# Kernel tuning notes

Measured on AMD Instinct MI355X. Metric: run time of the kernel, lower is better.

The kernel has to match this reference:

```python
import jax, jax.numpy as jnp
import numpy as np

DT = 0.1  # Euler timestep (init kwarg)

def setup_inputs() -> dict:
    key = jax.random.key(0)
    ks = jax.random.split(key, 6)
    B, L, S, U, H = 1024, 512, 64, 32, 512
    return {
        "initial_state": jax.random.normal(ks[0], (B, S), dtype=jnp.float32),
        "control_inputs": jax.random.normal(ks[1], (B, L, U), dtype=jnp.float32),
        "W1": jax.random.normal(ks[2], (S + U, H), dtype=jnp.float32) * (1.0 / np.sqrt(S + U)),
        "b1": jnp.zeros((H,), dtype=jnp.float32),
        "W2": jax.random.normal(ks[3], (H, S), dtype=jnp.float32) * (1.0 / np.sqrt(H)),
        "b2": jnp.zeros((S,), dtype=jnp.float32),
    }

def reference(initial_state, control_inputs, W1, b1, W2, b2):
    # Euler integration: state_{t+1} = state_t + dt * f(state_t, u_t)
    # f is a 2-layer tanh MLP on the concatenated [state, control].
    def step(state, u):
        z = jnp.concatenate([state, u], axis=-1)        # (B, S+U)
        diff = jnp.tanh(z @ W1 + b1) @ W2 + b2          # (B, S)
        new_state = state + diff * DT
        return new_state, new_state

    u_seq = jnp.swapaxes(control_inputs, 0, 1)          # (L, B, U)
    _, states = jax.lax.scan(step, initial_state, u_seq)  # (L, B, S)
    return jnp.swapaxes(states, 0, 1)                   # (B, L, S)
```

## Files before the change

### kernel.cpp

```cpp
#include <hip/hip_runtime.h>
#include <hip/hip_fp16.h>


typedef _Float16 f16;
typedef __attribute__((ext_vector_type(2))) _Float16 f16x2;
typedef __attribute__((ext_vector_type(8))) _Float16 f16x8;
typedef __attribute__((ext_vector_type(2))) float f32x2;
typedef __attribute__((ext_vector_type(4))) float f32x4;

#define MFMA16(a, b, c) __builtin_amdgcn_mfma_f32_16x16x32_f16((a), (b), (c), 0, 0, 0)

__device__ __forceinline__ f16x2 pkrtz(float a, float b) {
    return __builtin_bit_cast(f16x2, __builtin_amdgcn_cvt_pkrtz(a, b));
}

__device__ __forceinline__ float tanh_fast(float x) {
    float t = __builtin_amdgcn_exp2f(x * 2.885390081777927f);
    float r = __builtin_amdgcn_rcpf(t + 1.0f);
    return __builtin_fmaf(-2.0f, r, 1.0f);
}

__global__ __launch_bounds__(512, 1)
void euler_kernel(const float* __restrict__ init,
                  const float* __restrict__ uin,
                  const float* __restrict__ W1,
                  const float* __restrict__ b1,
                  const float* __restrict__ W2,
                  const float* __restrict__ b2,
                  float* __restrict__ out) {
    const int L = 512, S = 64, U = 32, H = 512;
    const int tid  = threadIdx.x;
    const int lane = tid & 63;
    const int w    = tid >> 6;
    const int g    = lane >> 4;
    const int r16  = lane & 15;
    const int b0   = blockIdx.x * 16;

    __shared__ f16   zbuf[256 * 8];
    __shared__ float pbuf[8 * 1024];

    f16x8 W1F[4][4];
    f16x8 W1Fu[2][4];
    #pragma unroll
    for (int kk = 0; kk < 6; ++kk)
      #pragma unroll
      for (int nf = 0; nf < 4; ++nf) {
          const int hcol = w * 64 + 32 * (nf >> 1) + 8 * (r16 >> 2) + 4 * (nf & 1) + (r16 & 3);
          #pragma unroll
          for (int j = 0; j < 8; ++j) {
              int k  = kk * 32 + g * 8 + j;
              int kr = (k < 128) ? (k & 63) : (64 + (k & 31));
              f16 v  = (f16)W1[kr * H + hcol];
              if (kk < 4) W1F[kk][nf][j] = v; else W1Fu[kk - 4][nf][j] = v;
          }
      }
    f32x4 b1v[4];
    #pragma unroll
    for (int nf = 0; nf < 4; ++nf)
        b1v[nf] = *(const f32x4*)&b1[w * 64 + 32 * (nf >> 1) + 4 * (nf & 1) + 8 * g];

    f16x8 W2F[2][4];
    #pragma unroll
    for (int a = 0; a < 2; ++a)
      #pragma unroll
      for (int ns = 0; ns < 4; ++ns)
        #pragma unroll
        for (int j = 0; j < 8; ++j) {
            int k = w * 64 + a * 32 + g * 8 + j;
            W2F[a][ns][j] = (f16)W2[k * S + ns * 16 + r16];
        }

    const int l5 = lane >> 5, r = lane & 31;
    const int sP = (w >> 1) * 16 + (r >> 1);
    const int bP = ((w & 1) * 2 + l5) * 4 + 2 * (r & 1);
    const float b2v = b2[sP];
    const int zci = ((sP >> 5) * 64 + ((sP >> 3) & 3) * 16 + bP) * 8 + (sP & 7);

    f32x2 stateF;
    stateF[0] = init[(size_t)(b0 + bP) * S + sP];
    stateF[1] = init[(size_t)(b0 + bP + 1) * S + sP];
    {
        f16x2 sh = pkrtz(stateF[0], stateF[1]);
        f16x2 sl = pkrtz(stateF[0] - (float)sh[0], stateF[1] - (float)sh[1]);
        zbuf[zci]            = sh[0];
        zbuf[zci + 8]        = sh[1];
        zbuf[zci + 1024]     = sl[0];
        zbuf[zci + 1024 + 8] = sl[1];
    }

    const float* uptr = uin + (size_t)(b0 + r16) * L * U + g * 8;
    f32x4 ua0 = *(const f32x4*)uptr;
    f32x4 ua1 = *(const f32x4*)(uptr + 4);
    f32x4 uacc[4];
    #pragma unroll
    for (int nf = 0; nf < 4; ++nf) uacc[nf] = b1v[nf];
    {
        f16x2 a01 = pkrtz(ua0[0], ua0[1]), a23 = pkrtz(ua0[2], ua0[3]);
        f16x2 c01 = pkrtz(ua1[0], ua1[1]), c23 = pkrtz(ua1[2], ua1[3]);
        f16x2 la  = pkrtz(ua0[0] - (float)a01[0], ua0[1] - (float)a01[1]);
        f16x2 lb  = pkrtz(ua0[2] - (float)a23[0], ua0[3] - (float)a23[1]);
        f16x2 lc  = pkrtz(ua1[0] - (float)c01[0], ua1[1] - (float)c01[1]);
        f16x2 ld  = pkrtz(ua1[2] - (float)c23[0], ua1[3] - (float)c23[1]);
        f16x8 uh, ul;
        uh[0]=a01[0]; uh[1]=a01[1]; uh[2]=a23[0]; uh[3]=a23[1];
        uh[4]=c01[0]; uh[5]=c01[1]; uh[6]=c23[0]; uh[7]=c23[1];
        ul[0]=la[0];  ul[1]=la[1];  ul[2]=lb[0];  ul[3]=lb[1];
        ul[4]=lc[0];  ul[5]=lc[1];  ul[6]=ld[0];  ul[7]=ld[1];
        #pragma unroll
        for (int nf = 0; nf < 4; ++nf) uacc[nf] = MFMA16(W1Fu[0][nf], uh, uacc[nf]);
        #pragma unroll
        for (int nf = 0; nf < 4; ++nf) uacc[nf] = MFMA16(W1Fu[1][nf], ul, uacc[nf]);
    }
    ua0 = *(const f32x4*)(uptr + U);
    ua1 = *(const f32x4*)(uptr + U + 4);
    __syncthreads();

    #pragma unroll 1
    for (int t = 0; t < L; ++t) {
        f16x8 zf[4];
        #pragma unroll
        for (int kk = 0; kk < 4; ++kk)
            zf[kk] = *(const f16x8*)&zbuf[(kk * 64 + lane) * 8];
        #pragma unroll
        for (int kk = 0; kk < 4; ++kk)
          #pragma unroll
          for (int nf = 0; nf < 4; ++nf)
            uacc[nf] = MFMA16(W1F[kk][nf], zf[kk], uacc[nf]);
        f16x8 hb[2];
        #pragma unroll
        for (int a = 0; a < 2; ++a)
          #pragma unroll
          for (int j8 = 0; j8 < 8; ++j8) {
              int nf = a * 2 + (j8 >> 2), jj = j8 & 3;
              hb[a][j8] = (f16)tanh_fast(uacc[nf][jj]);
          }
        f32x4 acc2[4];
        #pragma unroll
        for (int ns = 0; ns < 4; ++ns) acc2[ns] = (f32x4){0.f, 0.f, 0.f, 0.f};
        #pragma unroll
        for (int a = 0; a < 2; ++a)
          #pragma unroll
          for (int ns = 0; ns < 4; ++ns)
            acc2[ns] = MFMA16(hb[a], W2F[a][ns], acc2[ns]);
        #pragma unroll
        for (int ns = 0; ns < 4; ++ns)
            *(f32x4*)&pbuf[(w * 256 + ns * 64 + lane) * 4] = acc2[ns];

        #pragma unroll
        for (int nf = 0; nf < 4; ++nf) uacc[nf] = b1v[nf];
        {
            f16x2 a01 = pkrtz(ua0[0], ua0[1]), a23 = pkrtz(ua0[2], ua0[3]);
            f16x2 c01 = pkrtz(ua1[0], ua1[1]), c23 = pkrtz(ua1[2], ua1[3]);
            f16x2 la  = pkrtz(ua0[0] - (float)a01[0], ua0[1] - (float)a01[1]);
            f16x2 lb  = pkrtz(ua0[2] - (float)a23[0], ua0[3] - (float)a23[1]);
            f16x2 lc  = pkrtz(ua1[0] - (float)c01[0], ua1[1] - (float)c01[1]);
            f16x2 ld  = pkrtz(ua1[2] - (float)c23[0], ua1[3] - (float)c23[1]);
            f16x8 uh, ul;
            uh[0]=a01[0]; uh[1]=a01[1]; uh[2]=a23[0]; uh[3]=a23[1];
            uh[4]=c01[0]; uh[5]=c01[1]; uh[6]=c23[0]; uh[7]=c23[1];
            ul[0]=la[0];  ul[1]=la[1];  ul[2]=lb[0];  ul[3]=lb[1];
            ul[4]=lc[0];  ul[5]=lc[1];  ul[6]=ld[0];  ul[7]=ld[1];
            #pragma unroll
            for (int nf = 0; nf < 4; ++nf) uacc[nf] = MFMA16(W1Fu[0][nf], uh, uacc[nf]);
            #pragma unroll
            for (int nf = 0; nf < 4; ++nf) uacc[nf] = MFMA16(W1Fu[1][nf], ul, uacc[nf]);
        }
        {
            int tp = (t + 2 < L) ? (t + 2) : (L - 1);
            ua0 = *(const f32x4*)(uptr + (size_t)tp * U);
            ua1 = *(const f32x4*)(uptr + (size_t)tp * U + 4);
        }
        __syncthreads();

        f32x2 p[8];
        #pragma unroll
        for (int ww = 0; ww < 8; ++ww)
            p[ww] = *(const f32x2*)&pbuf[ww * 1024 + w * 128 + lane * 2];

        f32x2 s01 = (f32x2){0.f, 0.f}, s23 = s01, s45 = s01, s67 = s01;
        #pragma unroll
        for (int j = 0; j < 2; ++j) {
            s01[j] = p[0][j] + p[1][j];
            s23[j] = p[2][j] + p[3][j];
            s45[j] = p[4][j] + p[5][j];
            s67[j] = p[6][j] + p[7][j];
        }
        float d0 = ((s01[0] + s23[0]) + (s45[0] + s67[0])) + b2v;
        float d1 = ((s01[1] + s23[1]) + (s45[1] + s67[1])) + b2v;
        float sn0 = __builtin_fmaf(0.1f, d0, stateF[0]);
        float sn1 = __builtin_fmaf(0.1f, d1, stateF[1]);
        stateF[0] = sn0; stateF[1] = sn1;
        f16x2 sh = pkrtz(sn0, sn1);
        f16x2 sl = pkrtz(sn0 - (float)sh[0], sn1 - (float)sh[1]);
        zbuf[zci]            = sh[0];
        zbuf[zci + 8]        = sh[1];
        zbuf[zci + 1024]     = sl[0];
        zbuf[zci + 1024 + 8] = sl[1];
        out[((size_t)(b0 + bP) * L + t) * S + sP]     = sn0;
        out[((size_t)(b0 + bP + 1) * L + t) * S + sP] = sn1;
        __syncthreads();
    }
}

extern "C" void kernel_launch(void* const* d_in, const int* in_sizes, int n_in,
                              void* d_out, int out_size, void* d_ws, size_t ws_size,
                              hipStream_t stream) {
    const float* init = (const float*)d_in[0];
    const float* uin  = (const float*)d_in[1];
    const float* W1   = (const float*)d_in[2];
    const float* b1   = (const float*)d_in[3];
    const float* W2   = (const float*)d_in[4];
    const float* b2   = (const float*)d_in[5];
    euler_kernel<<<dim3(64), dim3(512), 0, stream>>>(init, uin, W1, b1, W2, b2,
                                                     (float*)d_out);
}
```

Before: 637.8 us.

## Stage control inputs through shared memory and fold U-projection into main MFMA chain

Previously every wave split the next control input into hi/lo fp16 parts and ran eight extra MFMAs for the U-part of layer 1 after the partial-sum store. Now only waves 6 and 7 convert the prefetched control input (hi and lo) and write it into two extra zbuf slots, and all waves treat it as two more K-chunks of the layer-1 MFMA chain. The final barrier is replaced by a manual waitcnt plus s_barrier. This removes per-wave duplicated conversion work and shortens the code between barriers, at the cost of a longer dependent MFMA chain on the critical path and a small load imbalance on waves 6 and 7.

After: 639.6 us. No clear change (+0.3%).

```diff
diff --git a/kernel.cpp b/kernel.cpp
--- a/kernel.cpp
+++ b/kernel.cpp
@@ -9,6 +9,10 @@
 typedef __attribute__((ext_vector_type(4))) float f32x4;
 
 #define MFMA16(a, b, c) __builtin_amdgcn_mfma_f32_16x16x32_f16((a), (b), (c), 0, 0, 0)
+
+#define BARB() do { asm volatile("s_waitcnt lgkmcnt(0)" ::: "memory"); \
+                    __builtin_amdgcn_s_barrier();                      \
+                    asm volatile("" ::: "memory"); } while (0)
 
 __device__ __forceinline__ f16x2 pkrtz(float a, float b) {
     return __builtin_bit_cast(f16x2, __builtin_amdgcn_cvt_pkrtz(a, b));
@@ -36,11 +40,10 @@
     const int r16  = lane & 15;
     const int b0   = blockIdx.x * 16;
 
-    __shared__ f16   zbuf[256 * 8];
+    __shared__ f16   zbuf[384 * 8];
     __shared__ float pbuf[8 * 1024];
 
-    f16x8 W1F[4][4];
-    f16x8 W1Fu[2][4];
+    f16x8 W1F[6][4];
     #pragma unroll
     for (int kk = 0; kk < 6; ++kk)
       #pragma unroll
@@ -50,8 +53,7 @@
           for (int j = 0; j < 8; ++j) {
               int k  = kk * 32 + g * 8 + j;
               int kr = (k < 128) ? (k & 63) : (64 + (k & 31));
-              f16 v  = (f16)W1[kr * H + hcol];
-              if (kk < 4) W1F[kk][nf][j] = v; else W1Fu[kk - 4][nf][j] = v;
+              W1F[kk][nf][j] = (f16)W1[kr * H + hcol];
           }
       }
     f32x4 b1v[4];
@@ -89,50 +91,55 @@
     }
 
     const float* uptr = uin + (size_t)(b0 + r16) * L * U + g * 8;
-    f32x4 ua0 = *(const f32x4*)uptr;
-    f32x4 ua1 = *(const f32x4*)(uptr + 4);
-    f32x4 uacc[4];
-    #pragma unroll
-    for (int nf = 0; nf < 4; ++nf) uacc[nf] = b1v[nf];
-    {
-        f16x2 a01 = pkrtz(ua0[0], ua0[1]), a23 = pkrtz(ua0[2], ua0[3]);
-        f16x2 c01 = pkrtz(ua1[0], ua1[1]), c23 = pkrtz(ua1[2], ua1[3]);
-        f16x2 la  = pkrtz(ua0[0] - (float)a01[0], ua0[1] - (float)a01[1]);
-        f16x2 lb  = pkrtz(ua0[2] - (float)a23[0], ua0[3] - (float)a23[1]);
-        f16x2 lc  = pkrtz(ua1[0] - (float)c01[0], ua1[1] - (float)c01[1]);
-        f16x2 ld  = pkrtz(ua1[2] - (float)c23[0], ua1[3] - (float)c23[1]);
-        f16x8 uh, ul;
-        uh[0]=a01[0]; uh[1]=a01[1]; uh[2]=a23[0]; uh[3]=a23[1];
-        uh[4]=c01[0]; uh[5]=c01[1]; uh[6]=c23[0]; uh[7]=c23[1];
-        ul[0]=la[0];  ul[1]=la[1];  ul[2]=lb[0];  ul[3]=lb[1];
-        ul[4]=lc[0];  ul[5]=lc[1];  ul[6]=ld[0];  ul[7]=ld[1];
-        #pragma unroll
-        for (int nf = 0; nf < 4; ++nf) uacc[nf] = MFMA16(W1Fu[0][nf], uh, uacc[nf]);
-        #pragma unroll
-        for (int nf = 0; nf < 4; ++nf) uacc[nf] = MFMA16(W1Fu[1][nf], ul, uacc[nf]);
+    f32x4 ua0 = (f32x4){0.f, 0.f, 0.f, 0.f}, ua1 = ua0;
+    if (w >= 6) {
+        f32x4 u0 = *(const f32x4*)uptr;
+        f32x4 u1 = *(const f32x4*)(uptr + 4);
+        f16x8 uv;
+        if (w == 6) {
+            f16x2 p01 = pkrtz(u0[0], u0[1]), p23 = pkrtz(u0[2], u0[3]);
+            f16x2 p45 = pkrtz(u1[0], u1[1]), p67 = pkrtz(u1[2], u1[3]);
+            uv[0]=p01[0]; uv[1]=p01[1]; uv[2]=p23[0]; uv[3]=p23[1];
+            uv[4]=p45[0]; uv[5]=p45[1]; uv[6]=p67[0]; uv[7]=p67[1];
+            *(f16x8*)&zbuf[(256 + lane) * 8] = uv;
+        } else {
+            f16x2 p01 = pkrtz(u0[0], u0[1]), p23 = pkrtz(u0[2], u0[3]);
+            f16x2 p45 = pkrtz(u1[0], u1[1]), p67 = pkrtz(u1[2], u1[3]);
+            f16x2 q01 = pkrtz(u0[0] - (float)p01[0], u0[1] - (float)p01[1]);
+            f16x2 q23 = pkrtz(u0[2] - (float)p23[0], u0[3] - (float)p23[1]);
+            f16x2 q45 = pkrtz(u1[0] - (float)p45[0], u1[1] - (float)p45[1]);
+            f16x2 q67 = pkrtz(u1[2] - (float)p67[0], u1[3] - (float)p67[1]);
+            uv[0]=q01[0]; uv[1]=q01[1]; uv[2]=q23[0]; uv[3]=q23[1];
+            uv[4]=q45[0]; uv[5]=q45[1]; uv[6]=q67[0]; uv[7]=q67[1];
+            *(f16x8*)&zbuf[(320 + lane) * 8] = uv;
+        }
+        ua0 = *(const f32x4*)(uptr + U);
+        ua1 = *(const f32x4*)(uptr + U + 4);
     }
-    ua0 = *(const f32x4*)(uptr + U);
-    ua1 = *(const f32x4*)(uptr + U + 4);
     __syncthreads();
 
     #pragma unroll 1
     for (int t = 0; t < L; ++t) {
-        f16x8 zf[4];
-        #pragma unroll
-        for (int kk = 0; kk < 4; ++kk)
+        f16x8 zf[6];
+        #pragma unroll
+        for (int kk = 0; kk < 6; ++kk)
             zf[kk] = *(const f16x8*)&zbuf[(kk * 64 + lane) * 8];
-        #pragma unroll
-        for (int kk = 0; kk < 4; ++kk)
+        f32x4 acc1[4];
+        #pragma unroll
+        for (int nf = 0; nf < 4; ++nf)
+            acc1[nf] = MFMA16(W1F[0][nf], zf[0], b1v[nf]);
+        #pragma unroll
+        for (int kk = 1; kk < 6; ++kk)
           #pragma unroll
           for (int nf = 0; nf < 4; ++nf)
-            uacc[nf] = MFMA16(W1F[kk][nf], zf[kk], uacc[nf]);
+            acc1[nf] = MFMA16(W1F[kk][nf], zf[kk], acc1[nf]);
         f16x8 hb[2];
         #pragma unroll
         for (int a = 0; a < 2; ++a)
           #pragma unroll
           for (int j8 = 0; j8 < 8; ++j8) {
               int nf = a * 2 + (j8 >> 2), jj = j8 & 3;
-              hb[a][j8] = (f16)tanh_fast(uacc[nf][jj]);
+              hb[a][j8] = (f16)tanh_fast(acc1[nf][jj]);
           }
         f32x4 acc2[4];
         #pragma unroll
@@ -145,37 +152,36 @@
         #pragma unroll
         for (int ns = 0; ns < 4; ++ns)
             *(f32x4*)&pbuf[(w * 256 + ns * 64 + lane) * 4] = acc2[ns];
-
-        #pragma unroll
-        for (int nf = 0; nf < 4; ++nf) uacc[nf] = b1v[nf];
-        {
-            f16x2 a01 = pkrtz(ua0[0], ua0[1]), a23 = pkrtz(ua0[2], ua0[3]);
-            f16x2 c01 = pkrtz(ua1[0], ua1[1]), c23 = pkrtz(ua1[2], ua1[3]);
-            f16x2 la  = pkrtz(ua0[0] - (float)a01[0], ua0[1] - (float)a01[1]);
-            f16x2 lb  = pkrtz(ua0[2] - (float)a23[0], ua0[3] - (float)a23[1]);
-            f16x2 lc  = pkrtz(ua1[0] - (float)c01[0], ua1[1] - (float)c01[1]);
-            f16x2 ld  = pkrtz(ua1[2] - (float)c23[0], ua1[3] - (float)c23[1]);
-            f16x8 uh, ul;
-            uh[0]=a01[0]; uh[1]=a01[1]; uh[2]=a23[0]; uh[3]=a23[1];
-            uh[4]=c01[0]; uh[5]=c01[1]; uh[6]=c23[0]; uh[7]=c23[1];
-            ul[0]=la[0];  ul[1]=la[1];  ul[2]=lb[0];  ul[3]=lb[1];
-            ul[4]=lc[0];  ul[5]=lc[1];  ul[6]=ld[0];  ul[7]=ld[1];
-            #pragma unroll
-            for (int nf = 0; nf < 4; ++nf) uacc[nf] = MFMA16(W1Fu[0][nf], uh, uacc[nf]);
-            #pragma unroll
-            for (int nf = 0; nf < 4; ++nf) uacc[nf] = MFMA16(W1Fu[1][nf], ul, uacc[nf]);
-        }
-        {
+        __syncthreads();
+
+        f32x2 p[8];
+        #pragma unroll
+        for (int ww = 0; ww < 8; ++ww)
+            p[ww] = *(const f32x2*)&pbuf[ww * 1024 + w * 128 + lane * 2];
+
+        if (w >= 6) {
+            if (t + 1 < L) {
+                f16x8 uv;
+                f16x2 p01 = pkrtz(ua0[0], ua0[1]), p23 = pkrtz(ua0[2], ua0[3]);
+                f16x2 p45 = pkrtz(ua1[0], ua1[1]), p67 = pkrtz(ua1[2], ua1[3]);
+                if (w == 6) {
+                    uv[0]=p01[0]; uv[1]=p01[1]; uv[2]=p23[0]; uv[3]=p23[1];
+                    uv[4]=p45[0]; uv[5]=p45[1]; uv[6]=p67[0]; uv[7]=p67[1];
+                    *(f16x8*)&zbuf[(256 + lane) * 8] = uv;
+                } else {
+                    f16x2 q01 = pkrtz(ua0[0] - (float)p01[0], ua0[1] - (float)p01[1]);
+                    f16x2 q23 = pkrtz(ua0[2] - (float)p23[0], ua0[3] - (float)p23[1]);
+                    f16x2 q45 = pkrtz(ua1[0] - (float)p45[0], ua1[1] - (float)p45[1]);
+                    f16x2 q67 = pkrtz(ua1[2] - (float)p67[0], ua1[3] - (float)p67[1]);
+                    uv[0]=q01[0]; uv[1]=q01[1]; uv[2]=q23[0]; uv[3]=q23[1];
+                    uv[4]=q45[0]; uv[5]=q45[1]; uv[6]=q67[0]; uv[7]=q67[1];
+                    *(f16x8*)&zbuf[(320 + lane) * 8] = uv;
+                }
+            }
             int tp = (t + 2 < L) ? (t + 2) : (L - 1);
             ua0 = *(const f32x4*)(uptr + (size_t)tp * U);
             ua1 = *(const f32x4*)(uptr + (size_t)tp * U + 4);
         }
-        __syncthreads();
-
-        f32x2 p[8];
-        #pragma unroll
-        for (int ww = 0; ww < 8; ++ww)
-            p[ww] = *(const f32x2*)&pbuf[ww * 1024 + w * 128 + lane * 2];
 
         f32x2 s01 = (f32x2){0.f, 0.f}, s23 = s01, s45 = s01, s67 = s01;
         #pragma unroll
@@ -198,7 +204,7 @@
         zbuf[zci + 1024 + 8] = sl[1];
         out[((size_t)(b0 + bP) * L + t) * S + sP]     = sn0;
         out[((size_t)(b0 + bP + 1) * L + t) * S + sP] = sn1;
-        __syncthreads();
+        BARB();
     }
 }
 
```
